# Kernel tuning notes

Measured on AMD Instinct MI355X. Metric: run time of the kernel, lower is better.

Reference implementation:

```python
import jax, jax.numpy as jnp
import numpy as np

DEG = 7
RANK = 8
B = 2_000_000

def setup_inputs() -> dict:
    key = jax.random.key(0)
    k_x, k0, k1, k2, k3 = jax.random.split(key, 5)
    d1 = DEG + 1
    # xavier_normal std = sqrt(2 / (fan_in + fan_out)); for 3D cores torch uses
    # fan_in = rank*(deg+1) style flattening, but any gaussian init is fine for a
    # numerical reference; use std matching 2D xavier on the (first, last) dims.
    def xavier(k, shape):
        fan_in, fan_out = shape[0], shape[-1]
        std = np.sqrt(2.0 / (fan_in + fan_out))
        return jax.random.normal(k, shape, dtype=jnp.float32) * std
    return {
        "X": jax.random.normal(k_x, (B, 4), dtype=jnp.float32),
        "G0": xavier(k0, (d1, RANK)),
        "G1": xavier(k1, (RANK, d1, RANK)),
        "G2": xavier(k2, (RANK, d1, RANK)),
        "G3": xavier(k3, (RANK, d1)),
    }

def reference(X, G0, G1, G2, G3):
    # poly bases: P[b, dim, p] = X[b, dim] ** p, p = 0..deg
    exps = jnp.arange(DEG + 1)               # [d1]
    P = X[:, :, None] ** exps                # [B, 4, d1]
    # chained TT contraction, left to right (avoids any large intermediate)
    t = jnp.einsum('bd,dr->br', P[:, 0], G0)           # [B, r]
    t = jnp.einsum('br,rds,bd->bs', t, G1, P[:, 1])    # [B, r]
    t = jnp.einsum('bs,sdt,bd->bt', t, G2, P[:, 2])    # [B, r]
    res = jnp.einsum('bt,td,bd->b', t, G3, P[:, 3])    # [B]
    return res.reshape(-1, 1)
```

## Files before the change

### kernel.cpp

```cpp
#include <hip/hip_runtime.h>
#include <hip/hip_bf16.h>

typedef float f32x4 __attribute__((ext_vector_type(4)));
typedef short bf16x8 __attribute__((ext_vector_type(8)));

__device__ inline unsigned cvt_pk_bf16(float a, float b) {
    unsigned r;
    asm("v_cvt_pk_bf16_f32 %0, %1, %2" : "=v"(r) : "v"(a), "v"(b));
    return r;
}
union FragU { unsigned u[4]; bf16x8 v; };

__device__ inline bf16x8 pack8(const float* f) {
    FragU x;
    x.u[0] = cvt_pk_bf16(f[0], f[1]);
    x.u[1] = cvt_pk_bf16(f[2], f[3]);
    x.u[2] = cvt_pk_bf16(f[4], f[5]);
    x.u[3] = cvt_pk_bf16(f[6], f[7]);
    return x.v;
}

__device__ inline void split_hl(const float* v, bf16x8& h8, bf16x8& l8) {
    float hi[8], lo[8];
    #pragma unroll
    for (int e = 0; e < 8; ++e) {
        float h = __bfloat162float(__float2bfloat16(v[e]));
        hi[e] = h; lo[e] = v[e] - h;
    }
    h8 = pack8(hi); l8 = pack8(lo);
}

__device__ inline float swz16_f(float v) {
    return __int_as_float(__builtin_amdgcn_ds_swizzle(__float_as_int(v), 0x401F));
}

#define POWERS(p, xx)                                              \
    p[0] = 1.f;  p[1] = (xx);      p[2] = p[1]*p[1];               \
    p[3] = p[2]*p[1]; p[4] = p[2]*p[2]; p[5] = p[4]*p[1];          \
    p[6] = p[4]*p[2]; p[7] = p[4]*p[3];

#define MFMA __builtin_amdgcn_mfma_f32_16x16x32_bf16

__global__ __launch_bounds__(256, 4) void tt_poly_kernel(
    const float* __restrict__ X,
    const float* __restrict__ G0,
    const float* __restrict__ G1,
    const float* __restrict__ G2,
    const float* __restrict__ G3,
    float* __restrict__ out,
    int B, int NW)
{
    const int tid   = threadIdx.x;
    const int lane  = tid & 63;
    const int row16 = lane & 15;
    const int quad  = lane >> 4;
    const int s8    = row16 & 7;
    const int gw    = blockIdx.x * 4 + (tid >> 6);

    bf16x8 A1h[2], A1l[2], A2h[2], A2l[2], A3h[2], A3l[2];
    #pragma unroll
    for (int q = 0; q < 2; ++q) {
        float v[8];
        #pragma unroll
        for (int e = 0; e < 8; ++e) {
            float a = 0.f;
            #pragma unroll
            for (int r = 0; r < 8; ++r)
                a = fmaf(G0[e*8 + r], G1[(r*8 + 4*q + quad)*8 + s8], a);
            v[e] = a;
        }
        split_hl(v, A1h[q], A1l[q]);
    }
    #pragma unroll
    for (int q = 0; q < 2; ++q) {
        float v[8];
        #pragma unroll
        for (int e = 0; e < 8; ++e)
            v[e] = G2[(e*8 + 4*q + quad)*8 + s8];
        split_hl(v, A2h[q], A2l[q]);
    }
    #pragma unroll
    for (int q = 0; q < 2; ++q) {
        float v[8];
        #pragma unroll
        for (int e = 0; e < 8; ++e)
            v[e] = G3[e*8 + 4*q + quad];
        split_hl(v, A3h[q], A3l[q]);
    }

    const bool oddq = (quad & 1) != 0;

    #pragma unroll 1
    for (int it = 0; it < 4; ++it) {
        const int sbase = (it * NW + gw) * 64;
        float resg[4];

        #pragma unroll
        for (int g4 = 0; g4 < 4; ++g4) {
            const int sidx = sbase + g4 * 16 + row16;
            float4 xs = (sidx < B) ? reinterpret_cast<const float4*>(X)[sidx]
                                   : make_float4(0.f, 0.f, 0.f, 0.f);

            float p0[8];
            POWERS(p0, xs.x)
            float x1sq = xs.y * xs.y, x1q4 = x1sq * x1sq;
            float sA = ((quad & 1) ? xs.y : 1.f) * ((quad & 2) ? x1sq : 1.f);
            float sB = sA * x1q4;
            float f0[8], f1[8];
            #pragma unroll
            for (int e = 0; e < 8; ++e) { f0[e] = p0[e] * sA; f1[e] = p0[e] * sB; }
            bf16x8 b0 = pack8(f0), b1 = pack8(f1);
            f32x4 ah = {0.f, 0.f, 0.f, 0.f}, al = {0.f, 0.f, 0.f, 0.f};
            ah = MFMA(A1h[0], b0, ah, 0, 0, 0);
            al = MFMA(A1l[0], b0, al, 0, 0, 0);
            ah = MFMA(A1h[1], b1, ah, 0, 0, 0);
            al = MFMA(A1l[1], b1, al, 0, 0, 0);
            f32x4 acc = ah + al;

            float t1v[8];
            {
                float sw0 = swz16_f(acc[0]), sw1 = swz16_f(acc[1]);
                float sw2 = swz16_f(acc[2]), sw3 = swz16_f(acc[3]);
                t1v[0] = oddq ? sw0 : acc[0];  t1v[4] = oddq ? acc[0] : sw0;
                t1v[1] = oddq ? sw1 : acc[1];  t1v[5] = oddq ? acc[1] : sw1;
                t1v[2] = oddq ? sw2 : acc[2];  t1v[6] = oddq ? acc[2] : sw2;
                t1v[3] = oddq ? sw3 : acc[3];  t1v[7] = oddq ? acc[3] : sw3;
            }

            float x2sq = xs.z * xs.z, x2q4 = x2sq * x2sq;
            float uA = ((quad & 1) ? xs.z : 1.f) * ((quad & 2) ? x2sq : 1.f);
            float uB = uA * x2q4;
            #pragma unroll
            for (int e = 0; e < 8; ++e) { f0[e] = t1v[e] * uA; f1[e] = t1v[e] * uB; }
            b0 = pack8(f0); b1 = pack8(f1);
            f32x4 bh = {0.f, 0.f, 0.f, 0.f}, bl = {0.f, 0.f, 0.f, 0.f};
            bh = MFMA(A2h[0], b0, bh, 0, 0, 0);
            bl = MFMA(A2l[0], b0, bl, 0, 0, 0);
            bh = MFMA(A2h[1], b1, bh, 0, 0, 0);
            bl = MFMA(A2l[1], b1, bl, 0, 0, 0);
            f32x4 acc2 = bh + bl;

            float t2v[8];
            {
                float sw0 = swz16_f(acc2[0]), sw1 = swz16_f(acc2[1]);
                float sw2 = swz16_f(acc2[2]), sw3 = swz16_f(acc2[3]);
                t2v[0] = oddq ? sw0 : acc2[0];  t2v[4] = oddq ? acc2[0] : sw0;
                t2v[1] = oddq ? sw1 : acc2[1];  t2v[5] = oddq ? acc2[1] : sw1;
                t2v[2] = oddq ? sw2 : acc2[2];  t2v[6] = oddq ? acc2[2] : sw2;
                t2v[3] = oddq ? sw3 : acc2[3];  t2v[7] = oddq ? acc2[3] : sw3;
            }

            float x3sq = xs.w * xs.w, x3q4 = x3sq * x3sq;
            float wA = ((quad & 1) ? xs.w : 1.f) * ((quad & 2) ? x3sq : 1.f);
            float wB = wA * x3q4;
            #pragma unroll
            for (int e = 0; e < 8; ++e) { f0[e] = t2v[e] * wA; f1[e] = t2v[e] * wB; }
            b0 = pack8(f0); b1 = pack8(f1);
            f32x4 ch = {0.f, 0.f, 0.f, 0.f}, cl = {0.f, 0.f, 0.f, 0.f};
            ch = MFMA(A3h[0], b0, ch, 0, 0, 0);
            cl = MFMA(A3l[0], b0, cl, 0, 0, 0);
            ch = MFMA(A3h[1], b1, ch, 0, 0, 0);
            cl = MFMA(A3l[1], b1, cl, 0, 0, 0);
            resg[g4] = ch[0] + cl[0];
        }

        float rv = (quad & 2) ? ((quad & 1) ? resg[3] : resg[2])
                              : ((quad & 1) ? resg[1] : resg[0]);
        const int b = sbase + lane;
        if (b < B) out[b] = rv;
    }
}

extern "C" void kernel_launch(void* const* d_in, const int* in_sizes, int n_in,
                              void* d_out, int out_size, void* d_ws, size_t ws_size,
                              hipStream_t stream) {
    const float* X  = (const float*)d_in[0];
    const float* G0 = (const float*)d_in[1];
    const float* G1 = (const float*)d_in[2];
    const float* G2 = (const float*)d_in[3];
    const float* G3 = (const float*)d_in[4];
    float* out = (float*)d_out;

    int B = in_sizes[0] / 4;
    int block = 256;
    int grid = (B + 1023) / 1024;
    int NW = grid * 4;
    tt_poly_kernel<<<grid, block, 0, stream>>>(X, G0, G1, G2, G3, out, B, NW);
}
```

Baseline: 45.40 us.

## Coalesce X loads with bpermute, drop final low-part MFMAs, use packed math

```diff
diff --git a/kernel.cpp b/kernel.cpp
--- a/kernel.cpp
+++ b/kernel.cpp
@@ -2,6 +2,7 @@
 #include <hip/hip_bf16.h>
 
 typedef float f32x4 __attribute__((ext_vector_type(4)));
+typedef float v2f  __attribute__((ext_vector_type(2)));
 typedef short bf16x8 __attribute__((ext_vector_type(8)));
 
 __device__ inline unsigned cvt_pk_bf16(float a, float b) {
@@ -19,6 +20,14 @@
     x.u[3] = cvt_pk_bf16(f[6], f[7]);
     return x.v;
 }
+__device__ inline bf16x8 pack8p(const v2f* f) {
+    FragU x;
+    x.u[0] = cvt_pk_bf16(f[0].x, f[0].y);
+    x.u[1] = cvt_pk_bf16(f[1].x, f[1].y);
+    x.u[2] = cvt_pk_bf16(f[2].x, f[2].y);
+    x.u[3] = cvt_pk_bf16(f[3].x, f[3].y);
+    return x.v;
+}
 
 __device__ inline void split_hl(const float* v, bf16x8& h8, bf16x8& l8) {
     float hi[8], lo[8];
@@ -30,6 +39,9 @@
     h8 = pack8(hi); l8 = pack8(lo);
 }
 
+__device__ inline float bperm_f(int idx_bytes, float v) {
+    return __int_as_float(__builtin_amdgcn_ds_bpermute(idx_bytes, __float_as_int(v)));
+}
 __device__ inline float swz16_f(float v) {
     return __int_as_float(__builtin_amdgcn_ds_swizzle(__float_as_int(v), 0x401F));
 }
@@ -40,8 +52,9 @@
     p[6] = p[4]*p[2]; p[7] = p[4]*p[3];
 
 #define MFMA __builtin_amdgcn_mfma_f32_16x16x32_bf16
-
-__global__ __launch_bounds__(256, 4) void tt_poly_kernel(
+#define IT 2
+
+__global__ __launch_bounds__(256, 2) void tt_poly_kernel(
     const float* __restrict__ X,
     const float* __restrict__ G0,
     const float* __restrict__ G1,
@@ -55,9 +68,18 @@
     const int row16 = lane & 15;
     const int quad  = lane >> 4;
     const int s8    = row16 & 7;
+    const int p     = quad & 1;
     const int gw    = blockIdx.x * 4 + (tid >> 6);
 
-    bf16x8 A1h[2], A1l[2], A2h[2], A2l[2], A3h[2], A3l[2];
+    float4 xva[IT];
+    #pragma unroll
+    for (int it = 0; it < IT; ++it) {
+        int b = (it * NW + gw) * 64 + lane;
+        xva[it] = (b < B) ? reinterpret_cast<const float4*>(X)[b]
+                          : make_float4(0.f, 0.f, 0.f, 0.f);
+    }
+
+    bf16x8 A1h[2], A1l[2], A2h[2], A2l[2], A3h[2];
     #pragma unroll
     for (int q = 0; q < 2; ++q) {
         float v[8];
@@ -75,93 +97,107 @@
     for (int q = 0; q < 2; ++q) {
         float v[8];
         #pragma unroll
-        for (int e = 0; e < 8; ++e)
-            v[e] = G2[(e*8 + 4*q + quad)*8 + s8];
+        for (int e = 0; e < 8; ++e) {
+            int su = p ? ((e + 4) & 7) : e;
+            v[e] = G2[(su*8 + 4*q + quad)*8 + s8];
+        }
         split_hl(v, A2h[q], A2l[q]);
     }
     #pragma unroll
     for (int q = 0; q < 2; ++q) {
         float v[8];
         #pragma unroll
-        for (int e = 0; e < 8; ++e)
-            v[e] = G3[e*8 + 4*q + quad];
-        split_hl(v, A3h[q], A3l[q]);
-    }
-
-    const bool oddq = (quad & 1) != 0;
-
-    #pragma unroll 1
-    for (int it = 0; it < 4; ++it) {
+        for (int e = 0; e < 8; ++e) {
+            int tu = p ? ((e + 4) & 7) : e;
+            v[e] = G3[tu*8 + 4*q + quad];
+        }
+        bf16x8 l8;
+        split_hl(v, A3h[q], l8);
+    }
+
+    #pragma unroll
+    for (int it = 0; it < IT; ++it) {
         const int sbase = (it * NW + gw) * 64;
+        const float4 xv = xva[it];
+
+        float x0g[4], x1g[4], x2g[4], x3g[4];
+        #pragma unroll
+        for (int g = 0; g < 4; ++g) {
+            const int src = (g * 16 + row16) * 4;
+            x0g[g] = bperm_f(src, xv.x);
+            x1g[g] = bperm_f(src, xv.y);
+            x2g[g] = bperm_f(src, xv.z);
+            x3g[g] = bperm_f(src, xv.w);
+        }
+
         float resg[4];
 
         #pragma unroll
         for (int g4 = 0; g4 < 4; ++g4) {
-            const int sidx = sbase + g4 * 16 + row16;
-            float4 xs = (sidx < B) ? reinterpret_cast<const float4*>(X)[sidx]
-                                   : make_float4(0.f, 0.f, 0.f, 0.f);
-
             float p0[8];
-            POWERS(p0, xs.x)
-            float x1sq = xs.y * xs.y, x1q4 = x1sq * x1sq;
-            float sA = ((quad & 1) ? xs.y : 1.f) * ((quad & 2) ? x1sq : 1.f);
+            POWERS(p0, x0g[g4])
+            float x1v = x1g[g4];
+            float x1sq = x1v * x1v, x1q4 = x1sq * x1sq;
+            float sA = (p ? x1v : 1.f) * ((quad & 2) ? x1sq : 1.f);
             float sB = sA * x1q4;
-            float f0[8], f1[8];
-            #pragma unroll
-            for (int e = 0; e < 8; ++e) { f0[e] = p0[e] * sA; f1[e] = p0[e] * sB; }
-            bf16x8 b0 = pack8(f0), b1 = pack8(f1);
-            f32x4 ah = {0.f, 0.f, 0.f, 0.f}, al = {0.f, 0.f, 0.f, 0.f};
-            ah = MFMA(A1h[0], b0, ah, 0, 0, 0);
-            al = MFMA(A1l[0], b0, al, 0, 0, 0);
+            v2f pr[4] = {{p0[0],p0[1]},{p0[2],p0[3]},{p0[4],p0[5]},{p0[6],p0[7]}};
+            v2f f0[4], f1[4];
+            v2f vA = {sA, sA}, vB = {sB, sB};
+            #pragma unroll
+            for (int j = 0; j < 4; ++j) { f0[j] = pr[j] * vA; f1[j] = pr[j] * vB; }
+            bf16x8 b0 = pack8p(f0), b1 = pack8p(f1);
+            f32x4 zh = {0.f,0.f,0.f,0.f};
+            f32x4 ah = MFMA(A1h[0], b0, zh, 0, 0, 0);
+            f32x4 al = MFMA(A1l[0], b0, zh, 0, 0, 0);
             ah = MFMA(A1h[1], b1, ah, 0, 0, 0);
             al = MFMA(A1l[1], b1, al, 0, 0, 0);
             f32x4 acc = ah + al;
 
-            float t1v[8];
+            v2f t1p[4];
             {
                 float sw0 = swz16_f(acc[0]), sw1 = swz16_f(acc[1]);
                 float sw2 = swz16_f(acc[2]), sw3 = swz16_f(acc[3]);
-                t1v[0] = oddq ? sw0 : acc[0];  t1v[4] = oddq ? acc[0] : sw0;
-                t1v[1] = oddq ? sw1 : acc[1];  t1v[5] = oddq ? acc[1] : sw1;
-                t1v[2] = oddq ? sw2 : acc[2];  t1v[6] = oddq ? acc[2] : sw2;
-                t1v[3] = oddq ? sw3 : acc[3];  t1v[7] = oddq ? acc[3] : sw3;
+                t1p[0] = (v2f){acc[0], acc[1]};
+                t1p[1] = (v2f){acc[2], acc[3]};
+                t1p[2] = (v2f){sw0, sw1};
+                t1p[3] = (v2f){sw2, sw3};
             }
 
-            float x2sq = xs.z * xs.z, x2q4 = x2sq * x2sq;
-            float uA = ((quad & 1) ? xs.z : 1.f) * ((quad & 2) ? x2sq : 1.f);
+            float x2v = x2g[g4];
+            float x2sq = x2v * x2v, x2q4 = x2sq * x2sq;
+            float uA = (p ? x2v : 1.f) * ((quad & 2) ? x2sq : 1.f);
             float uB = uA * x2q4;
-            #pragma unroll
-            for (int e = 0; e < 8; ++e) { f0[e] = t1v[e] * uA; f1[e] = t1v[e] * uB; }
-            b0 = pack8(f0); b1 = pack8(f1);
-            f32x4 bh = {0.f, 0.f, 0.f, 0.f}, bl = {0.f, 0.f, 0.f, 0.f};
-            bh = MFMA(A2h[0], b0, bh, 0, 0, 0);
-            bl = MFMA(A2l[0], b0, bl, 0, 0, 0);
+            v2f vU = {uA, uA}, vV = {uB, uB};
+            #pragma unroll
+            for (int j = 0; j < 4; ++j) { f0[j] = t1p[j] * vU; f1[j] = t1p[j] * vV; }
+            b0 = pack8p(f0); b1 = pack8p(f1);
+            f32x4 bh = MFMA(A2h[0], b0, zh, 0, 0, 0);
+            f32x4 bl = MFMA(A2l[0], b0, zh, 0, 0, 0);
             bh = MFMA(A2h[1], b1, bh, 0, 0, 0);
             bl = MFMA(A2l[1], b1, bl, 0, 0, 0);
             f32x4 acc2 = bh + bl;
 
-            float t2v[8];
+            v2f t2p[4];
             {
                 float sw0 = swz16_f(acc2[0]), sw1 = swz16_f(acc2[1]);
                 float sw2 = swz16_f(acc2[2]), sw3 = swz16_f(acc2[3]);
-                t2v[0] = oddq ? sw0 : acc2[0];  t2v[4] = oddq ? acc2[0] : sw0;
-                t2v[1] = oddq ? sw1 : acc2[1];  t2v[5] = oddq ? acc2[1] : sw1;
-                t2v[2] = oddq ? sw2 : acc2[2];  t2v[6] = oddq ? acc2[2] : sw2;
-                t2v[3] = oddq ? sw3 : acc2[3];  t2v[7] = oddq ? acc2[3] : sw3;
+                t2p[0] = (v2f){acc2[0], acc2[1]};
+                t2p[1] = (v2f){acc2[2], acc2[3]};
+                t2p[2] = (v2f){sw0, sw1};
+                t2p[3] = (v2f){sw2, sw3};
             }
 
-            float x3sq = xs.w * xs.w, x3q4 = x3sq * x3sq;
-            float wA = ((quad & 1) ? xs.w : 1.f) * ((quad & 2) ? x3sq : 1.f);
+            float x3v = x3g[g4];
+            float x3sq = x3v * x3v, x3q4 = x3sq * x3sq;
+            float wA = (p ? x3v : 1.f) * ((quad & 2) ? x3sq : 1.f);
             float wB = wA * x3q4;
-            #pragma unroll
-            for (int e = 0; e < 8; ++e) { f0[e] = t2v[e] * wA; f1[e] = t2v[e] * wB; }
-            b0 = pack8(f0); b1 = pack8(f1);
-            f32x4 ch = {0.f, 0.f, 0.f, 0.f}, cl = {0.f, 0.f, 0.f, 0.f};
-            ch = MFMA(A3h[0], b0, ch, 0, 0, 0);
-            cl = MFMA(A3l[0], b0, cl, 0, 0, 0);
-            ch = MFMA(A3h[1], b1, ch, 0, 0, 0);
-            cl = MFMA(A3l[1], b1, cl, 0, 0, 0);
-            resg[g4] = ch[0] + cl[0];
+            v2f vW = {wA, wA}, vZ = {wB, wB};
+            #pragma unroll
+            for (int j = 0; j < 4; ++j) { f0[j] = t2p[j] * vW; f1[j] = t2p[j] * vZ; }
+            b0 = pack8p(f0); b1 = pack8p(f1);
+            f32x4 acc3 = MFMA(A3h[0], b0, zh, 0, 0, 0);
+            acc3 = MFMA(A3h[1], b1, acc3, 0, 0, 0);
+            resg[g4] = acc3[0];
         }
 
         float rv = (quad & 2) ? ((quad & 1) ? resg[3] : resg[2])
@@ -183,7 +219,7 @@
 
     int B = in_sizes[0] / 4;
     int block = 256;
-    int grid = (B + 1023) / 1024;
+    int grid = (B + 64 * 4 * IT - 1) / (64 * 4 * IT);
     int NW = grid * 4;
     tt_poly_kernel<<<grid, block, 0, stream>>>(X, G0, G1, G2, G3, out, B, NW);
 }
```

New measurement: 40.44 us. 10.9% less time.
